# Kernel optimization log

Hardware: AMD Instinct MI355X
Metric: run time of the kernel (lower is better)

## Reference

```python
import jax, jax.numpy as jnp
import numpy as np

H = 8              # n_heads
N_PER_GRAPH = 64   # nodes per graph (equal-sized graphs)


def setup_inputs() -> dict:
    key = jax.random.key(0)
    ks = jax.random.split(key, 5)
    total, D = 65536, 512
    x = jax.random.normal(ks[0], (total, D), dtype=jnp.float32)
    batch = jnp.arange(total, dtype=jnp.int64) // N_PER_GRAPH  # sorted graph ids
    s = 1.0 / np.sqrt(D).astype(np.float32)
    # nn.MultiheadAttention packed in-proj (xavier-ish uniform) + zero bias
    in_proj_w = jax.random.uniform(ks[1], (3 * D, D), jnp.float32, -s, s)
    in_proj_b = jnp.zeros((3 * D,), jnp.float32)
    out_proj_w = jax.random.uniform(ks[2], (D, D), jnp.float32, -s, s)
    out_proj_b = jnp.zeros((D,), jnp.float32)
    gate_w = jax.random.uniform(ks[3], (1, D), jnp.float32, -s, s)
    gate_b = jnp.zeros((1,), jnp.float32)
    return {"x": x, "batch": batch, "in_proj_w": in_proj_w, "in_proj_b": in_proj_b,
            "out_proj_w": out_proj_w, "out_proj_b": out_proj_b,
            "gate_w": gate_w, "gate_b": gate_b}


def reference(x, batch, in_proj_w, in_proj_b, out_proj_w, out_proj_b, gate_w, gate_b):
    total, D = x.shape
    G = total // N_PER_GRAPH
    hd = D // H
    xg = x.reshape(G, N_PER_GRAPH, D)                       # [G, N, D]
    # packed qkv projection (torch: x @ in_proj_w.T + in_proj_b)
    qkv = jnp.einsum('gnd,ed->gne', xg, in_proj_w) + in_proj_b
    q, k, v = jnp.split(qkv, 3, axis=-1)
    def to_heads(t):
        return t.reshape(G, N_PER_GRAPH, H, hd).transpose(0, 2, 1, 3)  # [G, H, N, hd]
    q, k, v = to_heads(q), to_heads(k), to_heads(v)
    scores = jnp.einsum('ghnd,ghmd->ghnm', q, k) * (1.0 / np.sqrt(hd))
    attn = jax.nn.softmax(scores, axis=-1)
    ctx = jnp.einsum('ghnm,ghmd->ghnd', attn, v)
    ctx = ctx.transpose(0, 2, 1, 3).reshape(G, N_PER_GRAPH, D)
    attn_out = jnp.einsum('gnd,ed->gne', ctx, out_proj_w) + out_proj_b  # [G, N, D]
    gates = jax.nn.sigmoid(jnp.einsum('gnd,od->gno', attn_out, gate_w) + gate_b)
    return (attn_out * gates).sum(axis=1)                   # [G, D]
```

## Files before the change

kernel.cpp:

```cpp
#include <hip/hip_runtime.h>
#include <stdint.h>


typedef __attribute__((ext_vector_type(8))) short short8;
typedef __attribute__((ext_vector_type(4))) float f32x4;

#define D_ 512

#define WQKV_OFF   0u
#define WO_OFF     1572864u
#define UPART_OFF  2097152u
#define U_OFF      2129920u
#define C0_OFF     2131968u

__device__ __forceinline__ unsigned short f2bf(float f) {
    union { float f; unsigned int u; } t; t.f = f;
    unsigned int u = t.u;
    return (unsigned short)((u + 0x7FFFu + ((u >> 16) & 1u)) >> 16);
}
__device__ __forceinline__ unsigned pack2(float a, float b) {
    return (unsigned)f2bf(a) | ((unsigned)f2bf(b) << 16);
}
__device__ __forceinline__ float blo(unsigned v) {
    union { unsigned u; float f; } t; t.u = v << 16; return t.f;
}
__device__ __forceinline__ float bhi(unsigned v) {
    union { unsigned u; float f; } t; t.u = v & 0xFFFF0000u; return t.f;
}

__global__ __launch_bounds__(256)
void convert_and_u(const float* __restrict__ wqkv, const float* __restrict__ wo,
                   const float* __restrict__ gw,
                   unsigned short* __restrict__ wbf, float* __restrict__ upart) {
    const int b = blockIdx.x;
    const int t = threadIdx.x;
    if (b < 1024) {
        const int i4 = b * 256 + t;
        float4 v;
        if (i4 < 196608) v = *(const float4*)(wqkv + (size_t)i4 * 4);
        else             v = *(const float4*)(wo   + (size_t)(i4 - 196608) * 4);
        uint2 p; p.x = pack2(v.x, v.y); p.y = pack2(v.z, v.w);
        *(uint2*)(wbf + (size_t)i4 * 4) = p;
    } else {
        const int bb = b - 1024;
        float a0 = 0.f, a1 = 0.f;
        #pragma unroll 4
        for (int e = bb * 32; e < bb * 32 + 32; ++e) {
            const float ge = gw[e];
            a0 += wo[(size_t)e * 512 + t]       * ge;
            a1 += wo[(size_t)e * 512 + t + 256] * ge;
        }
        upart[bb * 512 + t] = a0; upart[bb * 512 + t + 256] = a1;
    }
}

__global__ __launch_bounds__(256)
void finalize_u(const float* __restrict__ upart, const float* __restrict__ bo,
                const float* __restrict__ gw, const float* __restrict__ gb,
                float* __restrict__ u, float* __restrict__ c0) {
    const int t = threadIdx.x;
    float s0 = 0.f, s1 = 0.f;
    #pragma unroll
    for (int b = 0; b < 16; ++b) { s0 += upart[b*512 + t]; s1 += upart[b*512 + t + 256]; }
    u[t] = s0; u[t + 256] = s1;
    __shared__ float rb[256];
    rb[t] = bo[t] * gw[t] + bo[t + 256] * gw[t + 256];
    __syncthreads();
    for (int s = 128; s > 0; s >>= 1) { if (t < s) rb[t] += rb[t + s]; __syncthreads(); }
    if (t == 0) c0[0] = rb[0] + gb[0];
}

union U8 { unsigned u[4]; short8 s; };

__global__ __launch_bounds__(512, 4)
void attn_full_kernel(const float* __restrict__ x,
                      const unsigned short* __restrict__ wqkv,
                      const float* __restrict__ bqkv,
                      const unsigned short* __restrict__ wo_bf,
                      const float* __restrict__ bo,
                      const float* __restrict__ u,
                      const float* __restrict__ c0,
                      float* __restrict__ out)
{
    __shared__ unsigned short xs[64][520];
    __shared__ float logitp[8][64];
    __shared__ float gatev[64];
    __shared__ float sgs;

    const int g    = blockIdx.x;
    const int tid  = threadIdx.x;
    const int w    = tid >> 6;
    const int lane = tid & 63;
    const int l15  = lane & 15;
    const int quad = lane >> 4;

    #pragma unroll
    for (int i = 0; i < 16; ++i) {
        int idx = tid + i * 512;
        int row = idx >> 7;
        int c4  = idx & 127;
        float4 v = *(const float4*)(x + ((size_t)(g*64 + row))*512 + c4*4);
        uint2 p; p.x = pack2(v.x, v.y); p.y = pack2(v.z, v.w);
        *(uint2*)(&xs[row][c4*4]) = p;
    }
    __syncthreads();

    const int h = w;

    U8 qA[4][2], kB[4][2];
    #pragma unroll
    for (int dt = 0; dt < 4; ++dt) {
        f32x4 aq[4], ak[4];
        #pragma unroll
        for (int nt = 0; nt < 4; ++nt) {
            aq[nt] = (f32x4){0.f,0.f,0.f,0.f};
            ak[nt] = (f32x4){0.f,0.f,0.f,0.f};
        }
        const unsigned short* wq = wqkv + (size_t)(       h*64 + dt*16 + l15) * 512;
        const unsigned short* wk = wqkv + (size_t)(512 +  h*64 + dt*16 + l15) * 512;
        #pragma unroll 4
        for (int ks = 0; ks < 16; ++ks) {
            const int col = ks*32 + quad*8;
            short8 a0 = *(const short8*)(wq + col);
            short8 a1 = *(const short8*)(wk + col);
            #pragma unroll
            for (int nt = 0; nt < 4; ++nt) {
                short8 b = *(const short8*)(&xs[nt*16 + l15][col]);
                aq[nt] = __builtin_amdgcn_mfma_f32_16x16x32_bf16(a0, b, aq[nt], 0,0,0);
                ak[nt] = __builtin_amdgcn_mfma_f32_16x16x32_bf16(a1, b, ak[nt], 0,0,0);
            }
        }
        float bq[4], bk2[4];
        #pragma unroll
        for (int r = 0; r < 4; ++r) {
            bq[r]  = bqkv[       h*64 + dt*16 + quad*4 + r];
            bk2[r] = bqkv[512 +  h*64 + dt*16 + quad*4 + r];
        }
        const bool take = ((quad >> 1) == (dt & 1));
        const int  ks2  = dt >> 1;
        #pragma unroll
        for (int nt = 0; nt < 4; ++nt) {
            unsigned q01 = pack2(aq[nt][0]+bq[0],  aq[nt][1]+bq[1]);
            unsigned q23 = pack2(aq[nt][2]+bq[2],  aq[nt][3]+bq[3]);
            unsigned k01 = pack2(ak[nt][0]+bk2[0], ak[nt][1]+bk2[1]);
            unsigned k23 = pack2(ak[nt][2]+bk2[2], ak[nt][3]+bk2[3]);
            #pragma unroll
            for (int j = 0; j < 4; ++j) {
                int srcl = ((quad & 1)*2 + (j >> 1))*16 + l15;
                unsigned tq = (unsigned)__shfl((int)((j & 1) ? q23 : q01), srcl);
                unsigned tk = (unsigned)__shfl((int)((j & 1) ? k23 : k01), srcl);
                if (take) { qA[nt][ks2].u[j] = tq; kB[nt][ks2].u[j] = tk; }
            }
        }
    }

    U8 pA[4][2];
    #pragma unroll
    for (int a = 0; a < 4; ++a) {
        f32x4 sc[4];
        #pragma unroll
        for (int b = 0; b < 4; ++b) sc[b] = (f32x4){0.f,0.f,0.f,0.f};
        #pragma unroll
        for (int ks2 = 0; ks2 < 2; ++ks2)
            #pragma unroll
            for (int b = 0; b < 4; ++b)
                sc[b] = __builtin_amdgcn_mfma_f32_16x16x32_bf16(
                            kB[b][ks2].s, qA[a][ks2].s, sc[b], 0,0,0);
        float m0 = -1e30f;
        #pragma unroll
        for (int b = 0; b < 4; ++b)
            #pragma unroll
            for (int r = 0; r < 4; ++r) { sc[b][r] *= 0.125f; m0 = fmaxf(m0, sc[b][r]); }
        m0 = fmaxf(m0, __shfl_xor(m0, 16));
        m0 = fmaxf(m0, __shfl_xor(m0, 32));
        float ssum = 0.f;
        #pragma unroll
        for (int b = 0; b < 4; ++b)
            #pragma unroll
            for (int r = 0; r < 4; ++r) { float e = __expf(sc[b][r] - m0); sc[b][r] = e; ssum += e; }
        ssum += __shfl_xor(ssum, 16);
        ssum += __shfl_xor(ssum, 32);
        float inv = 1.0f / ssum;
        unsigned pp[4][2];
        #pragma unroll
        for (int b = 0; b < 4; ++b) {
            pp[b][0] = pack2(sc[b][0]*inv, sc[b][1]*inv);
            pp[b][1] = pack2(sc[b][2]*inv, sc[b][3]*inv);
        }
        #pragma unroll
        for (int ks2 = 0; ks2 < 2; ++ks2)
            #pragma unroll
            for (int j = 0; j < 4; ++j) {
                int srcl = ((quad & 1)*2 + (j >> 1))*16 + l15;
                unsigned t0 = (unsigned)__shfl((int)pp[ks2*2    ][j & 1], srcl);
                unsigned t1 = (unsigned)__shfl((int)pp[ks2*2 + 1][j & 1], srcl);
                pA[a][ks2].u[j] = (quad >> 1) ? t1 : t0;
            }
    }

    f32x4 cacc[4][4];
    #pragma unroll
    for (int a = 0; a < 4; ++a)
        #pragma unroll
        for (int dt = 0; dt < 4; ++dt) cacc[a][dt] = (f32x4){0.f,0.f,0.f,0.f};
    #pragma unroll
    for (int dt = 0; dt < 4; ++dt) {
        f32x4 av[4];
        #pragma unroll
        for (int mt = 0; mt < 4; ++mt) av[mt] = (f32x4){0.f,0.f,0.f,0.f};
        const unsigned short* wv = wqkv + (size_t)(1024 + h*64 + dt*16 + l15) * 512;
        #pragma unroll 4
        for (int ks = 0; ks < 16; ++ks) {
            const int col = ks*32 + quad*8;
            short8 a2 = *(const short8*)(wv + col);
            #pragma unroll
            for (int mt = 0; mt < 4; ++mt) {
                short8 b = *(const short8*)(&xs[mt*16 + l15][col]);
                av[mt] = __builtin_amdgcn_mfma_f32_16x16x32_bf16(b, a2, av[mt], 0,0,0);
            }
        }
        const float bv = bqkv[1024 + h*64 + dt*16 + l15];
        unsigned vpk[4][2];
        #pragma unroll
        for (int mt = 0; mt < 4; ++mt) {
            vpk[mt][0] = pack2(av[mt][0]+bv, av[mt][1]+bv);
            vpk[mt][1] = pack2(av[mt][2]+bv, av[mt][3]+bv);
        }
        U8 vB[2];
        #pragma unroll
        for (int ks2 = 0; ks2 < 2; ++ks2)
            #pragma unroll
            for (int j = 0; j < 4; ++j) {
                int srcl = ((quad & 1)*2 + (j >> 1))*16 + l15;
                unsigned t0 = (unsigned)__shfl((int)vpk[ks2*2    ][j & 1], srcl);
                unsigned t1 = (unsigned)__shfl((int)vpk[ks2*2 + 1][j & 1], srcl);
                vB[ks2].u[j] = (quad >> 1) ? t1 : t0;
            }
        #pragma unroll
        for (int ks2 = 0; ks2 < 2; ++ks2)
            #pragma unroll
            for (int a = 0; a < 4; ++a)
                cacc[a][dt] = __builtin_amdgcn_mfma_f32_16x16x32_bf16(
                                  pA[a][ks2].s, vB[ks2].s, cacc[a][dt], 0,0,0);
    }

    {
        float ul[4];
        #pragma unroll
        for (int dt = 0; dt < 4; ++dt) ul[dt] = u[h*64 + dt*16 + l15];
        #pragma unroll
        for (int a = 0; a < 4; ++a)
            #pragma unroll
            for (int r = 0; r < 4; ++r) {
                float s = cacc[a][0][r]*ul[0] + cacc[a][1][r]*ul[1]
                        + cacc[a][2][r]*ul[2] + cacc[a][3][r]*ul[3];
                s += __shfl_xor(s, 1); s += __shfl_xor(s, 2);
                s += __shfl_xor(s, 4); s += __shfl_xor(s, 8);
                if (l15 == 0) logitp[w][a*16 + quad*4 + r] = s;
            }
    }
    __syncthreads();

    if (tid < 64) {
        float lg = c0[0];
        #pragma unroll
        for (int ww = 0; ww < 8; ++ww) lg += logitp[ww][tid];
        float gt = 1.0f / (1.0f + __expf(-lg));
        gatev[tid] = gt;
        float s = gt;
        s += __shfl_xor(s, 1);  s += __shfl_xor(s, 2);  s += __shfl_xor(s, 4);
        s += __shfl_xor(s, 8);  s += __shfl_xor(s, 16); s += __shfl_xor(s, 32);
        if (tid == 0) sgs = s;
    }
    __syncthreads();

    float* wctxs = (float*)&xs[0][0];
    {
        float4 gv[4];
        #pragma unroll
        for (int a = 0; a < 4; ++a) gv[a] = *(const float4*)&gatev[a*16 + quad*4];
        #pragma unroll
        for (int dt = 0; dt < 4; ++dt) {
            float s = 0.f;
            #pragma unroll
            for (int a = 0; a < 4; ++a) {
                s += cacc[a][dt][0]*gv[a].x + cacc[a][dt][1]*gv[a].y
                   + cacc[a][dt][2]*gv[a].z + cacc[a][dt][3]*gv[a].w;
            }
            s += __shfl_xor(s, 16); s += __shfl_xor(s, 32);
            if (quad == 0) wctxs[h*64 + dt*16 + l15] = s;
        }
    }
    __syncthreads();

    {
        const unsigned short* wr = wo_bf + (size_t)tid * 512;
        float acc = 0.f;
        #pragma unroll 8
        for (int i = 0; i < 64; ++i) {
            uint4  w4 = *(const uint4*)(wr + i*8);
            float4 ca = *(const float4*)(wctxs + i*8);
            float4 cb = *(const float4*)(wctxs + i*8 + 4);
            acc += blo(w4.x)*ca.x + bhi(w4.x)*ca.y + blo(w4.y)*ca.z + bhi(w4.y)*ca.w
                 + blo(w4.z)*cb.x + bhi(w4.z)*cb.y + blo(w4.w)*cb.z + bhi(w4.w)*cb.w;
        }
        out[(size_t)g*512 + tid] = acc + sgs * bo[tid];
    }
}

extern "C" void kernel_launch(void* const* d_in, const int* in_sizes, int n_in,
                              void* d_out, int out_size, void* d_ws, size_t ws_size,
                              hipStream_t stream) {
    const float* x    = (const float*)d_in[0];
    const float* wqkv = (const float*)d_in[2];
    const float* bqkv = (const float*)d_in[3];
    const float* wo   = (const float*)d_in[4];
    const float* bo   = (const float*)d_in[5];
    const float* gw   = (const float*)d_in[6];
    const float* gb   = (const float*)d_in[7];
    float* out = (float*)d_out;

    char* ws = (char*)d_ws;
    unsigned short* wqkv_bf = (unsigned short*)(ws + WQKV_OFF);
    unsigned short* wo_bf   = (unsigned short*)(ws + WO_OFF);
    float*          upart   = (float*)(ws + UPART_OFF);
    float*          u_ws    = (float*)(ws + U_OFF);
    float*          c0_ws   = (float*)(ws + C0_OFF);

    const int total = in_sizes[0] / D_;
    const int G     = total / 64;

    hipLaunchKernelGGL(convert_and_u, dim3(1040), dim3(256), 0, stream,
                       wqkv, wo, gw, wqkv_bf, upart);
    hipLaunchKernelGGL(finalize_u,    dim3(1),    dim3(256), 0, stream,
                       upart, bo, gw, gb, u_ws, c0_ws);
    hipLaunchKernelGGL(attn_full_kernel, dim3(G), dim3(512), 0, stream,
                       x, wqkv_bf, bqkv, wo_bf, bo, u_ws, c0_ws, out);
}
```

Measured before the change: 452.2 us.

## Reassociate ctx products to skip P·V MFMAs, using matrix-vector contractions instead

Rather than forming the full context tile P·V with MFMAs and then contracting with u and the gate weights, the kernel first contracts V with u (V·u) and P with the gates (gᵀP), then finishes with small dot products and cross-lane shuffle reductions. This drops the 32 P·V MFMA instructions per wave along with the 64-float accumulator array. In exchange it keeps all V fragments live in registers and adds many scalar bf16 unpacks and shuffle reductions. Results should match up to rounding, since the reassociation is exact in real arithmetic.

Measured after the change: 491.1 us. 8.6% more time.

```diff
diff --git a/kernel.cpp b/kernel.cpp
--- a/kernel.cpp
+++ b/kernel.cpp
@@ -198,11 +198,12 @@
             }
     }
 
-    f32x4 cacc[4][4];
-    #pragma unroll
-    for (int a = 0; a < 4; ++a)
-        #pragma unroll
-        for (int dt = 0; dt < 4; ++dt) cacc[a][dt] = (f32x4){0.f,0.f,0.f,0.f};
+    U8 vB[4][2];
+    float ym[2][8];
+    #pragma unroll
+    for (int ks2 = 0; ks2 < 2; ++ks2)
+        #pragma unroll
+        for (int m = 0; m < 8; ++m) ym[ks2][m] = 0.f;
     #pragma unroll
     for (int dt = 0; dt < 4; ++dt) {
         f32x4 av[4];
@@ -226,7 +227,6 @@
             vpk[mt][0] = pack2(av[mt][0]+bv, av[mt][1]+bv);
             vpk[mt][1] = pack2(av[mt][2]+bv, av[mt][3]+bv);
         }
-        U8 vB[2];
         #pragma unroll
         for (int ks2 = 0; ks2 < 2; ++ks2)
             #pragma unroll
@@ -234,30 +234,41 @@
                 int srcl = ((quad & 1)*2 + (j >> 1))*16 + l15;
                 unsigned t0 = (unsigned)__shfl((int)vpk[ks2*2    ][j & 1], srcl);
                 unsigned t1 = (unsigned)__shfl((int)vpk[ks2*2 + 1][j & 1], srcl);
-                vB[ks2].u[j] = (quad >> 1) ? t1 : t0;
-            }
-        #pragma unroll
-        for (int ks2 = 0; ks2 < 2; ++ks2)
-            #pragma unroll
-            for (int a = 0; a < 4; ++a)
-                cacc[a][dt] = __builtin_amdgcn_mfma_f32_16x16x32_bf16(
-                                  pA[a][ks2].s, vB[ks2].s, cacc[a][dt], 0,0,0);
-    }
-
-    {
-        float ul[4];
-        #pragma unroll
-        for (int dt = 0; dt < 4; ++dt) ul[dt] = u[h*64 + dt*16 + l15];
-        #pragma unroll
-        for (int a = 0; a < 4; ++a)
-            #pragma unroll
-            for (int r = 0; r < 4; ++r) {
-                float s = cacc[a][0][r]*ul[0] + cacc[a][1][r]*ul[1]
-                        + cacc[a][2][r]*ul[2] + cacc[a][3][r]*ul[3];
-                s += __shfl_xor(s, 1); s += __shfl_xor(s, 2);
-                s += __shfl_xor(s, 4); s += __shfl_xor(s, 8);
-                if (l15 == 0) logitp[w][a*16 + quad*4 + r] = s;
-            }
+                vB[dt][ks2].u[j] = (quad >> 1) ? t1 : t0;
+            }
+        const float ulv = u[h*64 + dt*16 + l15];
+        #pragma unroll
+        for (int ks2 = 0; ks2 < 2; ++ks2)
+            #pragma unroll
+            for (int j = 0; j < 4; ++j) {
+                unsigned vv = vB[dt][ks2].u[j];
+                ym[ks2][2*j]   += blo(vv) * ulv;
+                ym[ks2][2*j+1] += bhi(vv) * ulv;
+            }
+    }
+    #pragma unroll
+    for (int ks2 = 0; ks2 < 2; ++ks2)
+        #pragma unroll
+        for (int m = 0; m < 8; ++m) {
+            float v = ym[ks2][m];
+            v += __shfl_xor(v, 1); v += __shfl_xor(v, 2);
+            v += __shfl_xor(v, 4); v += __shfl_xor(v, 8);
+            ym[ks2][m] = v;
+        }
+
+    #pragma unroll
+    for (int a = 0; a < 4; ++a) {
+        float lg = 0.f;
+        #pragma unroll
+        for (int ks2 = 0; ks2 < 2; ++ks2)
+            #pragma unroll
+            for (int j = 0; j < 4; ++j) {
+                unsigned pv = pA[a][ks2].u[j];
+                lg += blo(pv) * ym[ks2][2*j] + bhi(pv) * ym[ks2][2*j+1];
+            }
+        lg += __shfl_xor(lg, 16);
+        lg += __shfl_xor(lg, 32);
+        if (quad == 0) logitp[w][a*16 + l15] = lg;
     }
     __syncthreads();
 
@@ -276,18 +287,44 @@
 
     float* wctxs = (float*)&xs[0][0];
     {
-        float4 gv[4];
-        #pragma unroll
-        for (int a = 0; a < 4; ++a) gv[a] = *(const float4*)&gatev[a*16 + quad*4];
+        float gl[4];
+        #pragma unroll
+        for (int a = 0; a < 4; ++a) gl[a] = gatev[a*16 + l15];
+        float tm[2][8];
+        #pragma unroll
+        for (int ks2 = 0; ks2 < 2; ++ks2)
+            #pragma unroll
+            for (int j = 0; j < 4; ++j) {
+                float t0 = 0.f, t1 = 0.f;
+                #pragma unroll
+                for (int a = 0; a < 4; ++a) {
+                    unsigned pv = pA[a][ks2].u[j];
+                    t0 += blo(pv) * gl[a];
+                    t1 += bhi(pv) * gl[a];
+                }
+                tm[ks2][2*j] = t0; tm[ks2][2*j+1] = t1;
+            }
+        #pragma unroll
+        for (int ks2 = 0; ks2 < 2; ++ks2)
+            #pragma unroll
+            for (int m = 0; m < 8; ++m) {
+                float v = tm[ks2][m];
+                v += __shfl_xor(v, 1); v += __shfl_xor(v, 2);
+                v += __shfl_xor(v, 4); v += __shfl_xor(v, 8);
+                tm[ks2][m] = v;
+            }
         #pragma unroll
         for (int dt = 0; dt < 4; ++dt) {
             float s = 0.f;
             #pragma unroll
-            for (int a = 0; a < 4; ++a) {
-                s += cacc[a][dt][0]*gv[a].x + cacc[a][dt][1]*gv[a].y
-                   + cacc[a][dt][2]*gv[a].z + cacc[a][dt][3]*gv[a].w;
-            }
-            s += __shfl_xor(s, 16); s += __shfl_xor(s, 32);
+            for (int ks2 = 0; ks2 < 2; ++ks2)
+                #pragma unroll
+                for (int j = 0; j < 4; ++j) {
+                    unsigned vv = vB[dt][ks2].u[j];
+                    s += blo(vv) * tm[ks2][2*j] + bhi(vv) * tm[ks2][2*j+1];
+                }
+            s += __shfl_xor(s, 16);
+            s += __shfl_xor(s, 32);
             if (quad == 0) wctxs[h*64 + dt*16 + l15] = s;
         }
     }
```
